# Kernel tuning notes

Hardware: AMD Instinct MI355X
Metric: run time of the kernel (lower is better)

## Reference

```python
import jax, jax.numpy as jnp
import numpy as np

HIDDEN = 4096
NH = 32        # num attention heads
NKV = 8        # num key/value heads
HD = 128       # q/k head dim
VHD = 96       # v head dim
ROT = 64       # rotary dim = int(HD * 0.5)
THETA = 10000.0
B, S = 2, 2048


def setup_inputs() -> dict:
    key = jax.random.key(0)
    ks = jax.random.split(key, 6)
    w = 0.02
    return {
        "hidden_states": jax.random.normal(ks[0], (B, S, HIDDEN), jnp.float32),
        "position_ids": jnp.arange(B * S, dtype=jnp.int32).reshape(B, S) % S,
        "Wq": jax.random.normal(ks[1], (NH * HD, HIDDEN), jnp.float32) * w,
        "Wk": jax.random.normal(ks[2], (NKV * HD, HIDDEN), jnp.float32) * w,
        "Wv": jax.random.normal(ks[3], (NKV * VHD, HIDDEN), jnp.float32) * w,
        "Wo": jax.random.normal(ks[4], (HIDDEN, NH * VHD), jnp.float32) * w,
    }


def _rotate_half(x):
    x1, x2 = x[..., : x.shape[-1] // 2], x[..., x.shape[-1] // 2 :]
    return jnp.concatenate((-x2, x1), axis=-1)


def reference(hidden_states, position_ids, Wq, Wk, Wv, Wo):
    b, s, _ = hidden_states.shape
    # QKV projections (torch Linear: y = x @ W^T)
    q = (hidden_states @ Wq.T).reshape(b, s, NH, HD).transpose(0, 2, 1, 3)   # [b,NH,s,HD]
    k = (hidden_states @ Wk.T).reshape(b, s, NKV, HD).transpose(0, 2, 1, 3)  # [b,NKV,s,HD]
    v = (hidden_states @ Wv.T).reshape(b, s, NKV, VHD).transpose(0, 2, 1, 3)  # [b,NKV,s,VHD]

    # rotary embedding over first ROT dims (partial RoPE)
    inv_freq = 1.0 / (THETA ** (jnp.arange(0, ROT, 2, dtype=jnp.float32) / ROT))  # [ROT/2]
    freqs = position_ids.astype(jnp.float32)[:, :, None] * inv_freq              # [b,s,ROT/2]
    emb = jnp.concatenate((freqs, freqs), axis=-1)                                # [b,s,ROT]
    cos = jnp.cos(emb)[:, None, :, :].astype(hidden_states.dtype)                 # [b,1,s,ROT]
    sin = jnp.sin(emb)[:, None, :, :].astype(hidden_states.dtype)

    q_rot, q_pass = q[..., :ROT], q[..., ROT:]
    k_rot, k_pass = k[..., :ROT], k[..., ROT:]
    q_rot = q_rot * cos + _rotate_half(q_rot) * sin
    k_rot = k_rot * cos + _rotate_half(k_rot) * sin
    q = jnp.concatenate((q_rot, q_pass), axis=-1)
    k = jnp.concatenate((k_rot, k_pass), axis=-1)

    # GQA: repeat_kv (repeat_interleave over head dim)
    n_rep = NH // NKV
    k = jnp.repeat(k, n_rep, axis=1)  # [b,NH,s,HD]
    v = jnp.repeat(v, n_rep, axis=1)  # [b,NH,s,VHD]

    scores = jnp.einsum("bhqd,bhkd->bhqk", q, k) / np.float32(np.sqrt(HD))
    # causal additive mask (attention_mask as built by the HF model)
    neg = jnp.finfo(jnp.float32).min
    causal = jnp.where(jnp.tril(jnp.ones((s, s), dtype=bool)), 0.0, neg)
    scores = scores + causal[None, None, :, :]

    attn = jax.nn.softmax(scores.astype(jnp.float32), axis=-1).astype(q.dtype)
    out = jnp.einsum("bhqk,bhkd->bhqd", attn, v)          # [b,NH,s,VHD]
    out = out.transpose(0, 2, 1, 3).reshape(b, s, NH * VHD)
    return out @ Wo.T                                      # [b,s,HIDDEN]
```

## Files before the change

kernel.cpp:

```cpp
#include <hip/hip_runtime.h>

typedef __attribute__((ext_vector_type(4))) float f32x4;
typedef __attribute__((ext_vector_type(8))) __bf16 bf16x8;
typedef __attribute__((ext_vector_type(8))) unsigned short u16x8;
typedef __attribute__((ext_vector_type(4))) unsigned short u16x4;
typedef __attribute__((ext_vector_type(4))) short s16x4;
typedef unsigned short ushort_t;

__device__ __forceinline__ unsigned short f2bf(float x) {
  unsigned u = __builtin_bit_cast(unsigned, x);
  u += 0x7fffu + ((u >> 16) & 1u);
  return (unsigned short)(u >> 16);
}
__device__ __forceinline__ float bf2f(unsigned short h) {
  unsigned u = ((unsigned)h) << 16;
  return __builtin_bit_cast(float, u);
}
__device__ __forceinline__ short f2bf_n(float x) {
  return __builtin_bit_cast(short, (__bf16)x);
}

__device__ __forceinline__ void gload_lds16(const void* g, void* l) {
  __builtin_amdgcn_global_load_lds(
      (const __attribute__((address_space(1))) unsigned int*)g,
      (__attribute__((address_space(3))) unsigned int*)l, 16, 0, 0);
}

__global__ __launch_bounds__(256) void k_f32_to_bf16(
    const float* __restrict__ src, ushort_t* __restrict__ dst, int n8) {
  int i = blockIdx.x * 256 + threadIdx.x;
  if (i >= n8) return;
  float4 a = ((const float4*)src)[i * 2 + 0];
  float4 b = ((const float4*)src)[i * 2 + 1];
  u16x8 o;
  o[0] = f2bf(a.x); o[1] = f2bf(a.y); o[2] = f2bf(a.z); o[3] = f2bf(a.w);
  o[4] = f2bf(b.x); o[5] = f2bf(b.y); o[6] = f2bf(b.z); o[7] = f2bf(b.w);
  ((u16x8*)dst)[i] = o;
}

__global__ __launch_bounds__(256) void k_rope(
    ushort_t* __restrict__ QKV, const int* __restrict__ pos_ids) {
  int idx = blockIdx.x * 256 + threadIdx.x;
  if (idx >= 4096 * 40 * 32) return;
  int d = idx & 31;
  int rem = idx >> 5;
  int hh = rem % 40;
  int tk = rem / 40;
  int pos = pos_ids[tk];
  float inv = exp2f(-(float)d * (13.287712379549449f / 32.0f));
  float ang = (float)pos * inv;
  float s, c;
  __sincosf(ang, &s, &c);
  int col = (hh < 32) ? (hh * 128 + d) : (4096 + (hh - 32) * 128 + d);
  ushort_t* p = QKV + (size_t)tk * 5888 + col;
  float x1 = bf2f(p[0]);
  float x2 = bf2f(p[32]);
  p[0]  = f2bf(x1 * c - x2 * s);
  p[32] = f2bf(x2 * c + x1 * s);
}

template <int OUT_BF16>
__global__ __launch_bounds__(512, 2) void k_gemm8(
    const ushort_t* __restrict__ A, const ushort_t* __restrict__ B,
    void* __restrict__ C, int K, int lda, int ldb, int ldc) {
  __shared__ ushort_t lds[3][(128 + 256) * 64];
  const int t = threadIdx.x;
  const int w = t >> 6, ln = t & 63;
  const int fr = ln & 15, fg = ln >> 4;
  const int wm = w >> 2, wn = w & 3;
  const int m0 = blockIdx.x * 128, n0 = blockIdx.y * 256;

  const int srow = t >> 3;
  const int scolb = ((t & 7) * 16) ^ ((srow & 7) << 4);
  const ushort_t* pA = A + (size_t)(m0 + srow) * lda + (scolb >> 1);
  const ushort_t* pB = B + (size_t)(n0 + srow) * ldb + (scolb >> 1);

  f32x4 acc[4][4] = {};

  const int nt = K >> 6;

#define STAGE(bufi, k0)                                                       \
  {                                                                           \
    char* d_ = (char*)&lds[(bufi)][0];                                        \
    _Pragma("unroll") for (int i_ = 0; i_ < 2; ++i_)                          \
        gload_lds16(pA + (size_t)i_ * 64 * lda + (k0),                        \
                    d_ + i_ * 8192 + t * 16);                                 \
    char* dB_ = d_ + 16384;                                                   \
    _Pragma("unroll") for (int i_ = 0; i_ < 4; ++i_)                          \
        gload_lds16(pB + (size_t)i_ * 64 * ldb + (k0),                        \
                    dB_ + i_ * 8192 + t * 16);                                \
  }

  STAGE(0, 0)
  STAGE(1, 64)
  asm volatile("s_waitcnt vmcnt(6)" ::: "memory");
  __builtin_amdgcn_s_barrier();
  asm volatile("" ::: "memory");

  for (int kt = 0; kt < nt; ++kt) {
    const int cur = kt % 3;
    if (kt + 2 < nt) STAGE((kt + 2) % 3, (kt + 2) << 6)
    const char* bA = (const char*)&lds[cur][0];
    const char* bB = bA + 16384;

    bf16x8 af[4][2];
#pragma unroll
    for (int m = 0; m < 4; ++m) {
      const int r = wm * 64 + m * 16 + fr;
#pragma unroll
      for (int kk = 0; kk < 2; ++kk)
        af[m][kk] = *(const bf16x8*)(bA + r * 128 +
                                     ((kk * 64 + fg * 16) ^ ((r & 7) << 4)));
    }
    {
      bf16x8 bfv[2][2];
#pragma unroll
      for (int n = 0; n < 2; ++n) {
        const int r = wn * 64 + n * 16 + fr;
#pragma unroll
        for (int kk = 0; kk < 2; ++kk)
          bfv[n][kk] = *(const bf16x8*)(bB + r * 128 +
                                        ((kk * 64 + fg * 16) ^ ((r & 7) << 4)));
      }
      __builtin_amdgcn_s_setprio(1);
#pragma unroll
      for (int m = 0; m < 4; ++m)
#pragma unroll
        for (int n = 0; n < 2; ++n)
#pragma unroll
          for (int kk = 0; kk < 2; ++kk)
            acc[m][n] = __builtin_amdgcn_mfma_f32_16x16x32_bf16(
                af[m][kk], bfv[n][kk], acc[m][n], 0, 0, 0);
      __builtin_amdgcn_s_setprio(0);
    }
    {
      bf16x8 bfv[2][2];
#pragma unroll
      for (int n = 0; n < 2; ++n) {
        const int r = wn * 64 + (n + 2) * 16 + fr;
#pragma unroll
        for (int kk = 0; kk < 2; ++kk)
          bfv[n][kk] = *(const bf16x8*)(bB + r * 128 +
                                        ((kk * 64 + fg * 16) ^ ((r & 7) << 4)));
      }
      __builtin_amdgcn_s_setprio(1);
#pragma unroll
      for (int m = 0; m < 4; ++m)
#pragma unroll
        for (int n = 0; n < 2; ++n)
#pragma unroll
          for (int kk = 0; kk < 2; ++kk)
            acc[m][n + 2] = __builtin_amdgcn_mfma_f32_16x16x32_bf16(
                af[m][kk], bfv[n][kk], acc[m][n + 2], 0, 0, 0);
      __builtin_amdgcn_s_setprio(0);
    }
    if (kt + 1 < nt) {
      __builtin_amdgcn_sched_barrier(0);
      if (kt + 2 < nt)
        asm volatile("s_waitcnt vmcnt(6)" ::: "memory");
      else
        asm volatile("s_waitcnt vmcnt(0)" ::: "memory");
      __builtin_amdgcn_s_barrier();
      asm volatile("" ::: "memory");
    }
  }
#undef STAGE

#pragma unroll
  for (int m = 0; m < 4; ++m)
#pragma unroll
    for (int n = 0; n < 4; ++n) {
      const int row = m0 + wm * 64 + m * 16 + fg * 4;
      const int col = n0 + wn * 64 + n * 16 + fr;
#pragma unroll
      for (int j = 0; j < 4; ++j) {
        if (OUT_BF16)
          ((ushort_t*)C)[(size_t)(row + j) * ldc + col] = f2bf(acc[m][n][j]);
        else
          ((float*)C)[(size_t)(row + j) * ldc + col] = acc[m][n][j];
      }
    }
}

__global__ __launch_bounds__(256, 2) void k_attn(
    const ushort_t* __restrict__ QKV, ushort_t* __restrict__ O) {
  __shared__ ushort_t lK[64 * 128];
  __shared__ ushort_t lV[16 * 96 * 4];

  const int t = threadIdx.x, ln = t & 63, w = t >> 6;
  const int fr = ln & 15, fg = ln >> 4;
  const int h = blockIdx.y, b = blockIdx.z;
  const int qt = ((h >> 4) & 1) ? (15 - (int)blockIdx.x) : (int)blockIdx.x;
  const int hk = h >> 2;
  const int q0 = qt * 128 + w * 32;
  const int tb = b * 2048;

  bf16x8 qf[2][4];
#pragma unroll
  for (int rq = 0; rq < 2; ++rq)
#pragma unroll
    for (int kb = 0; kb < 4; ++kb)
      qf[rq][kb] = *(const bf16x8*)(QKV +
                    (size_t)(tb + q0 + rq * 16 + fr) * 5888 + h * 128 +
                    kb * 32 + fg * 8);

  f32x4 oacc[6][2] = {};
  float mreg[2] = {-1e30f, -1e30f};
  float lreg[2] = {0.f, 0.f};

  const int krow = t >> 4;
  const int kse = ((((t & 15) * 16) ^ (((t >> 4) & 7) << 4)) >> 1);
  const int k4s = t / 12, c8s = t % 12;

  const float sc = 0.088388347648318447f;
  const float l2e = 1.4426950408889634f;
  const float scl2e = sc * l2e;

  const int nkt = (qt + 1) * 2;
  for (int kt = 0; kt < nkt; ++kt) {
    const int kb0 = kt * 64;
    __syncthreads();
    {
      const ushort_t* pK =
          QKV + (size_t)(tb + kb0 + krow) * 5888 + 4096 + hk * 128 + kse;
#pragma unroll
      for (int i = 0; i < 4; ++i)
        gload_lds16(pK + (size_t)i * 16 * 5888,
                    (char*)lK + i * 4096 + (w << 10));
    }
    if (t < 192) {
      const ushort_t* pV =
          QKV + (size_t)(tb + kb0 + k4s * 4) * 5888 + 5120 + hk * 96 + c8s * 8;
      u16x8 vrow[4];
#pragma unroll
      for (int kr = 0; kr < 4; ++kr)
        vrow[kr] = *(const u16x8*)(pV + (size_t)kr * 5888);
#pragma unroll
      for (int i = 0; i < 8; ++i) {
        int cs = (c8s * 8 + i) ^ (k4s & 15);
        u16x4 q;
#pragma unroll
        for (int kr = 0; kr < 4; ++kr) q[kr] = vrow[kr][i];
        *(u16x4*)(&lV[(k4s * 96 + cs) * 4]) = q;
      }
    }
    __syncthreads();
    if (kb0 > q0 + 31) continue;
    f32x4 s[4][2] = {};
    __builtin_amdgcn_s_setprio(1);
#pragma unroll
    for (int cb = 0; cb < 4; ++cb) {
      const int kv = cb * 16 + fr;
      bf16x8 kf[4];
#pragma unroll
      for (int kb = 0; kb < 4; ++kb)
        kf[kb] = *(const bf16x8*)((const char*)lK + kv * 256 +
                                  ((kb * 64 + fg * 16) ^ ((kv & 7) << 4)));
#pragma unroll
      for (int rq = 0; rq < 2; ++rq)
#pragma unroll
        for (int kb = 0; kb < 4; ++kb)
          s[cb][rq] = __builtin_amdgcn_mfma_f32_16x16x32_bf16(
              kf[kb], qf[rq][kb], s[cb][rq], 0, 0, 0);
    }
    __builtin_amdgcn_s_setprio(0);
    if (kb0 + 63 > q0) {
#pragma unroll
      for (int rq = 0; rq < 2; ++rq) {
        const int qrel = q0 + rq * 16 + fr - kb0;
#pragma unroll
        for (int cb = 0; cb < 4; ++cb)
#pragma unroll
          for (int j = 0; j < 4; ++j)
            if (cb * 16 + fg * 4 + j > qrel) s[cb][rq][j] = -3.0e38f;
      }
    }
    float pmax[2];
#pragma unroll
    for (int rq = 0; rq < 2; ++rq) {
      f32x4 rm4 = s[0][rq];
#pragma unroll
      for (int cb = 1; cb < 4; ++cb)
#pragma unroll
        for (int j = 0; j < 4; ++j) rm4[j] = fmaxf(rm4[j], s[cb][rq][j]);
      float rm = fmaxf(fmaxf(rm4[0], rm4[1]), fmaxf(rm4[2], rm4[3]));
      rm = fmaxf(rm, __shfl_xor(rm, 16, 64));
      rm = fmaxf(rm, __shfl_xor(rm, 32, 64));
      pmax[rq] = rm * sc;
    }
    bool need = (pmax[0] > mreg[0] + 6.f) || (pmax[1] > mreg[1] + 6.f);
    if (__any(need)) {
#pragma unroll
      for (int rq = 0; rq < 2; ++rq) {
        float mnew = fmaxf(mreg[rq], pmax[rq]);
        float sf = exp2f((mreg[rq] - mnew) * l2e);
        mreg[rq] = mnew;
        lreg[rq] *= sf;
#pragma unroll
        for (int c6 = 0; c6 < 6; ++c6) oacc[c6][rq] *= sf;
      }
    }
    s16x4 pb[4][2];
#pragma unroll
    for (int rq = 0; rq < 2; ++rq) {
      const float mb = mreg[rq] * l2e;
      f32x4 ps4 = {};
#pragma unroll
      for (int cb = 0; cb < 4; ++cb) {
#pragma unroll
        for (int j = 0; j < 4; ++j) {
          float p = exp2f(fmaf(s[cb][rq][j], scl2e, -mb));
          s[cb][rq][j] = p;
          ps4[j] += p;
        }
      }
      float ps = (ps4[0] + ps4[1]) + (ps4[2] + ps4[3]);
      ps += __shfl_xor(ps, 16, 64);
      ps += __shfl_xor(ps, 32, 64);
      lreg[rq] += ps;
#pragma unroll
      for (int cb = 0; cb < 4; ++cb) {
        s16x4 v;
#pragma unroll
        for (int j = 0; j < 4; ++j) v[j] = f2bf_n(s[cb][rq][j]);
        pb[cb][rq] = v;
      }
    }
    __builtin_amdgcn_s_setprio(1);
#pragma unroll
    for (int cb = 0; cb < 4; ++cb) {
      const int k4 = cb * 4 + fg;
      s16x4 va[6];
#pragma unroll
      for (int c6 = 0; c6 < 6; ++c6)
        va[c6] = *(const s16x4*)(
            &lV[(k4 * 96 + (((c6 * 16 + fr) ^ (k4 & 15)))) * 4]);
#pragma unroll
      for (int c6 = 0; c6 < 6; ++c6)
#pragma unroll
        for (int rq = 0; rq < 2; ++rq)
          oacc[c6][rq] = __builtin_amdgcn_mfma_f32_16x16x16bf16_1k(
              va[c6], pb[cb][rq], oacc[c6][rq], 0, 0, 0);
    }
    __builtin_amdgcn_s_setprio(0);
  }
#pragma unroll
  for (int rq = 0; rq < 2; ++rq) {
    const float inv = 1.0f / lreg[rq];
    const size_t rowb = (size_t)(tb + q0 + rq * 16 + fr) * 3072 + h * 96;
#pragma unroll
    for (int c6 = 0; c6 < 6; ++c6) {
      u16x4 o;
#pragma unroll
      for (int j = 0; j < 4; ++j)
        o[j] = (unsigned short)f2bf_n(oacc[c6][rq][j] * inv);
      *(u16x4*)(&O[rowb + c6 * 16 + fg * 4]) = o;
    }
  }
}

extern "C" void kernel_launch(void* const* d_in, const int* in_sizes, int n_in,
                              void* d_out, int out_size, void* d_ws,
                              size_t ws_size, hipStream_t stream) {
  const float* X  = (const float*)d_in[0];
  const int*   pos = (const int*)d_in[1];
  const float* Wq = (const float*)d_in[2];
  const float* Wk = (const float*)d_in[3];
  const float* Wv = (const float*)d_in[4];
  const float* Wo = (const float*)d_in[5];
  float* out = (float*)d_out;

  ushort_t* Xb    = (ushort_t*)d_ws;
  ushort_t* Wob   = Xb + 16777216;
  ushort_t* QKV   = Wob + 12582912;
  ushort_t* AO    = QKV + 24117248;
  ushort_t* Wqkvb = (ushort_t*)d_out;

  k_f32_to_bf16<<<8192, 256, 0, stream>>>(X, Xb, 2097152);
  k_f32_to_bf16<<<8192, 256, 0, stream>>>(Wq, Wqkvb, 2097152);
  k_f32_to_bf16<<<2048, 256, 0, stream>>>(Wk, Wqkvb + 16777216, 524288);
  k_f32_to_bf16<<<1536, 256, 0, stream>>>(Wv, Wqkvb + 20971520, 393216);
  k_f32_to_bf16<<<6144, 256, 0, stream>>>(Wo, Wob, 1572864);

  k_gemm8<1><<<dim3(32, 23), 512, 0, stream>>>(Xb, Wqkvb, QKV, 4096, 4096,
                                               4096, 5888);
  k_rope<<<20480, 256, 0, stream>>>(QKV, pos);
  k_attn<<<dim3(16, 32, 2), 256, 0, stream>>>(QKV, AO);
  k_gemm8<0><<<dim3(32, 16), 512, 0, stream>>>(AO, Wob, out, 3072, 3072,
                                               3072, 4096);
}
```

Before: 517.5 us.

## Split GEMM main loop into barrier-separated phases interleaving loads with MFMA

Restructures the GEMM k-loop into four phases. Each phase issues one third of the next-stage global-to-LDS prefetch, a subset of the LDS fragment reads, and a 2x2 quadrant of MFMAs, with a workgroup barrier between phases. The aim is to spread memory issue across the compute so loads overlap MFMA work better, similar to ping-pong scheduling. In exchange it adds three extra barriers per iteration, which can stall waves if the phases are unbalanced.

```diff
diff --git a/kernel.cpp b/kernel.cpp
--- a/kernel.cpp
+++ b/kernel.cpp
@@ -76,95 +76,101 @@
   const ushort_t* pB = B + (size_t)(n0 + srow) * ldb + (scolb >> 1);
 
   f32x4 acc[4][4] = {};
-
   const int nt = K >> 6;
 
-#define STAGE(bufi, k0)                                                       \
+#define STAGE_P(bufi, k0, part)                                               \
   {                                                                           \
     char* d_ = (char*)&lds[(bufi)][0];                                        \
-    _Pragma("unroll") for (int i_ = 0; i_ < 2; ++i_)                          \
-        gload_lds16(pA + (size_t)i_ * 64 * lda + (k0),                        \
-                    d_ + i_ * 8192 + t * 16);                                 \
-    char* dB_ = d_ + 16384;                                                   \
-    _Pragma("unroll") for (int i_ = 0; i_ < 4; ++i_)                          \
-        gload_lds16(pB + (size_t)i_ * 64 * ldb + (k0),                        \
-                    dB_ + i_ * 8192 + t * 16);                                \
-  }
-
-  STAGE(0, 0)
-  STAGE(1, 64)
+    if ((part) == 0) {                                                        \
+      gload_lds16(pA + (k0), d_ + t * 16);                                    \
+      gload_lds16(pA + (size_t)64 * lda + (k0), d_ + 8192 + t * 16);          \
+    } else if ((part) == 1) {                                                 \
+      gload_lds16(pB + (k0), d_ + 16384 + t * 16);                            \
+      gload_lds16(pB + (size_t)64 * ldb + (k0), d_ + 24576 + t * 16);         \
+    } else {                                                                  \
+      gload_lds16(pB + (size_t)128 * ldb + (k0), d_ + 32768 + t * 16);        \
+      gload_lds16(pB + (size_t)192 * ldb + (k0), d_ + 40960 + t * 16);        \
+    }                                                                         \
+  }
+
+#define LD_A(mi)                                                              \
+  {                                                                           \
+    const int r_ = wm * 64 + (mi)*16 + fr;                                    \
+    af[mi][0] = *(const bf16x8*)(bA + r_ * 128 +                              \
+                                 ((fg * 16) ^ ((r_ & 7) << 4)));              \
+    af[mi][1] = *(const bf16x8*)(bA + r_ * 128 +                              \
+                                 ((64 + fg * 16) ^ ((r_ & 7) << 4)));         \
+  }
+#define LD_B(ni)                                                              \
+  {                                                                           \
+    const int r_ = wn * 64 + (ni)*16 + fr;                                    \
+    bfv[ni][0] = *(const bf16x8*)(bB + r_ * 128 +                             \
+                                  ((fg * 16) ^ ((r_ & 7) << 4)));             \
+    bfv[ni][1] = *(const bf16x8*)(bB + r_ * 128 +                             \
+                                  ((64 + fg * 16) ^ ((r_ & 7) << 4)));        \
+  }
+#define MFMA_Q(ms, ns)                                                        \
+  {                                                                           \
+    __builtin_amdgcn_s_setprio(1);                                            \
+    _Pragma("unroll") for (int m_ = 0; m_ < 2; ++m_)                          \
+        _Pragma("unroll") for (int n_ = 0; n_ < 2; ++n_)                      \
+            _Pragma("unroll") for (int kk_ = 0; kk_ < 2; ++kk_)               \
+                acc[(ms) + m_][(ns) + n_] =                                   \
+                    __builtin_amdgcn_mfma_f32_16x16x32_bf16(                  \
+                        af[(ms) + m_][kk_], bfv[(ns) + n_][kk_],              \
+                        acc[(ms) + m_][(ns) + n_], 0, 0, 0);                  \
+    __builtin_amdgcn_s_setprio(0);                                            \
+  }
+#define PHASE_BAR()                                                           \
+  {                                                                           \
+    __builtin_amdgcn_s_barrier();                                             \
+    asm volatile("" ::: "memory");                                            \
+    __builtin_amdgcn_sched_barrier(0);                                        \
+  }
+
+  STAGE_P(0, 0, 0) STAGE_P(0, 0, 1) STAGE_P(0, 0, 2)
+  STAGE_P(1, 64, 0) STAGE_P(1, 64, 1) STAGE_P(1, 64, 2)
   asm volatile("s_waitcnt vmcnt(6)" ::: "memory");
   __builtin_amdgcn_s_barrier();
   asm volatile("" ::: "memory");
 
   for (int kt = 0; kt < nt; ++kt) {
-    const int cur = kt % 3;
-    if (kt + 2 < nt) STAGE((kt + 2) % 3, (kt + 2) << 6)
-    const char* bA = (const char*)&lds[cur][0];
+    const char* bA = (const char*)&lds[kt % 3][0];
     const char* bB = bA + 16384;
-
-    bf16x8 af[4][2];
-#pragma unroll
-    for (int m = 0; m < 4; ++m) {
-      const int r = wm * 64 + m * 16 + fr;
-#pragma unroll
-      for (int kk = 0; kk < 2; ++kk)
-        af[m][kk] = *(const bf16x8*)(bA + r * 128 +
-                                     ((kk * 64 + fg * 16) ^ ((r & 7) << 4)));
-    }
-    {
-      bf16x8 bfv[2][2];
-#pragma unroll
-      for (int n = 0; n < 2; ++n) {
-        const int r = wn * 64 + n * 16 + fr;
-#pragma unroll
-        for (int kk = 0; kk < 2; ++kk)
-          bfv[n][kk] = *(const bf16x8*)(bB + r * 128 +
-                                        ((kk * 64 + fg * 16) ^ ((r & 7) << 4)));
-      }
-      __builtin_amdgcn_s_setprio(1);
-#pragma unroll
-      for (int m = 0; m < 4; ++m)
-#pragma unroll
-        for (int n = 0; n < 2; ++n)
-#pragma unroll
-          for (int kk = 0; kk < 2; ++kk)
-            acc[m][n] = __builtin_amdgcn_mfma_f32_16x16x32_bf16(
-                af[m][kk], bfv[n][kk], acc[m][n], 0, 0, 0);
-      __builtin_amdgcn_s_setprio(0);
-    }
-    {
-      bf16x8 bfv[2][2];
-#pragma unroll
-      for (int n = 0; n < 2; ++n) {
-        const int r = wn * 64 + (n + 2) * 16 + fr;
-#pragma unroll
-        for (int kk = 0; kk < 2; ++kk)
-          bfv[n][kk] = *(const bf16x8*)(bB + r * 128 +
-                                        ((kk * 64 + fg * 16) ^ ((r & 7) << 4)));
-      }
-      __builtin_amdgcn_s_setprio(1);
-#pragma unroll
-      for (int m = 0; m < 4; ++m)
-#pragma unroll
-        for (int n = 0; n < 2; ++n)
-#pragma unroll
-          for (int kk = 0; kk < 2; ++kk)
-            acc[m][n + 2] = __builtin_amdgcn_mfma_f32_16x16x32_bf16(
-                af[m][kk], bfv[n][kk], acc[m][n + 2], 0, 0, 0);
-      __builtin_amdgcn_s_setprio(0);
-    }
+    const bool pre = (kt + 2 < nt);
+    const int pbuf = (kt + 2) % 3;
+    const int pk = (kt + 2) << 6;
+    bf16x8 af[4][2], bfv[4][2];
+
+    if (pre) STAGE_P(pbuf, pk, 0)
+    LD_A(0) LD_A(1) LD_B(0) LD_B(1)
+    MFMA_Q(0, 0)
+    PHASE_BAR()
+    if (pre) STAGE_P(pbuf, pk, 1)
+    LD_B(2) LD_B(3)
+    MFMA_Q(0, 2)
+    PHASE_BAR()
+    if (pre) STAGE_P(pbuf, pk, 2)
+    LD_A(2) LD_A(3)
+    MFMA_Q(2, 0)
+    PHASE_BAR()
+    MFMA_Q(2, 2)
     if (kt + 1 < nt) {
       __builtin_amdgcn_sched_barrier(0);
-      if (kt + 2 < nt)
+      if (pre)
         asm volatile("s_waitcnt vmcnt(6)" ::: "memory");
       else
         asm volatile("s_waitcnt vmcnt(0)" ::: "memory");
       __builtin_amdgcn_s_barrier();
       asm volatile("" ::: "memory");
-    }
-  }
-#undef STAGE
+      __builtin_amdgcn_sched_barrier(0);
+    }
+  }
+#undef STAGE_P
+#undef LD_A
+#undef LD_B
+#undef MFMA_Q
+#undef PHASE_BAR
 
 #pragma unroll
   for (int m = 0; m < 4; ++m)
```

After: 526.3 us. No clear change (+1.7%).
